# Performance work log

Measured on AMD Instinct MI355X. Metric: run time of the kernel, lower is better.

The kernel has to match this reference:

```python
import jax, jax.numpy as jnp
import numpy as np

SEM_DIM = 256
N_LEVELS = 21
HALF = jnp.float32((N_LEVELS - 1) / 2.0)  # 10.0
BETA = 0.1  # commitment cost


def setup_inputs() -> dict:
    key = jax.random.key(0)
    k1, k2 = jax.random.split(key)
    z = jax.random.normal(k1, (8, 292, 2048), dtype=jnp.float32)
    # nn.init.uniform_(codebook.weight, -1/dim, 1/dim)
    codebook = jax.random.uniform(k2, (8192, SEM_DIM), dtype=jnp.float32,
                                  minval=-1.0 / SEM_DIM, maxval=1.0 / SEM_DIM)
    return {"z": z, "codebook": codebook}


def reference(z, codebook):
    # Split latent: semantic (VQ) / acoustic (FSQ)
    z_sem = z[:, :SEM_DIM, :]   # (B, 256, T)
    z_ac = z[:, SEM_DIM:, :]    # (B, 36, T)
    B, D, T = z_sem.shape

    # ---- VectorQuantizer (eval path) ----
    z_flat = jnp.transpose(z_sem, (0, 2, 1)).reshape(B * T, D)  # (BT, D)
    # ||z||^2 - 2 z.c^T + ||c||^2
    dists = (jnp.sum(z_flat * z_flat, axis=1, keepdims=True)
             - 2.0 * jnp.einsum('nd,kd->nk', z_flat, codebook)
             + jnp.sum(codebook * codebook, axis=1)[None, :])  # (BT, K)
    indices = jnp.argmin(dists, axis=1)  # (BT,)
    z_q = codebook[indices].reshape(B, T, D).transpose(0, 2, 1)  # (B, D, T)

    codebook_loss = jnp.mean((z_q - jax.lax.stop_gradient(z_sem)) ** 2)
    commitment_loss = BETA * jnp.mean((jax.lax.stop_gradient(z_q) - z_sem) ** 2)
    vq_loss = codebook_loss + commitment_loss

    # straight-through
    z_sem_q = z_sem + jax.lax.stop_gradient(z_q - z_sem)

    # ---- FSQ quantize (eval path) ----
    z_b = jnp.tanh(z_ac) * HALF
    z_ac_q = z_b + jax.lax.stop_gradient(jnp.round(z_b) - z_b)  # round STE
    ac_codes = jnp.clip(jnp.round(z_ac_q + HALF).astype(jnp.int32), 0, N_LEVELS - 1)

    z_out = jnp.concatenate([z_sem_q, z_ac_q], axis=1)  # (B, 292, T)
    return z_out, indices.reshape(B, T), ac_codes, vq_loss, z_ac_q
```

## Files before the change

### kernel.cpp

```cpp
#include <hip/hip_runtime.h>
#include <cfloat>
#include <math.h>

#define BQ 8
#define T 2048
#define D 256
#define DAC 36
#define CH 292
#define K 8192
#define NROWS (BQ*T)
#define TAU 1e-3f
#define FSPLIT 4
#define RSPLIT 16
#define CAPROWS 8192

#define OFF_IDX   (BQ*CH*T)
#define OFF_CODES (OFF_IDX + NROWS)
#define OFF_LOSS  (OFF_CODES + BQ*DAC*T)
#define OFF_ACQ   (OFF_LOSS + 1)

#define WN_C2    0
#define WN_Z2    32768
#define WN_CNT   98304
#define WN_LIST  98560
#define WN_LOSS  164096
#define WN_WIDX  168192
#define WN_QCNT  233728
#define WN_PMX   262144
#define WN_PR    262144
#define WN_AZ    2359296
#define WN_ZG    2359296
#define WN_BC    10747904
#define WN_QL    14942208
#define WN_NEED  15204352

#define WS_C2    0
#define WS_Z2    32768
#define WS_PART  131072
#define WS_IDX   655360
#define WS_LOSS  720896
#define MT 32
#define KT 128
#define DC 32
#define NSPLIT 4

typedef float f32x4 __attribute__((ext_vector_type(4)));
typedef __bf16 bf16x8 __attribute__((ext_vector_type(8)));
typedef __attribute__((address_space(1))) const unsigned int gu32;
typedef __attribute__((address_space(3))) unsigned int lu32;

__device__ inline void gl_lds16(const void* gp, void* lp) {
    __builtin_amdgcn_global_load_lds((gu32*)gp, (lu32*)lp, 16, 0, 0);
}

__device__ inline unsigned short f2bf(float x) {
    unsigned u = __float_as_uint(x);
    return (unsigned short)((u + 0x7fffu + ((u >> 16) & 1u)) >> 16);
}

__device__ inline void merge3(float& m1, float& m2, int& mi, float o1, float o2, int oi) {
    if (o1 < m1 || (o1 == m1 && oi < mi)) { m2 = fminf(m1, o2); m1 = o1; mi = oi; }
    else                                  { m2 = fminf(m2, o1); }
}

template <typename F>
__device__ float np_pairwise256_sq(F ld) {
    float S[2];
    #pragma unroll
    for (int h = 0; h < 2; h++) {
        int base = h * 128;
        float v[16];
        #pragma unroll
        for (int l = 0; l < 16; l++) {
            float q[8];
            #pragma unroll
            for (int j = 0; j < 8; j++) { float x = ld(base + j * 16 + l); q[j] = x * x; }
            v[l] = ((q[0] + q[1]) + (q[2] + q[3])) + ((q[4] + q[5]) + (q[6] + q[7]));
        }
        float t1[8], t2[4], t3[2];
        #pragma unroll
        for (int l = 0; l < 8; l++) t1[l] = v[l] + v[l + 8];
        #pragma unroll
        for (int l = 0; l < 4; l++) t2[l] = t1[l] + t1[l + 4];
        t3[0] = t2[0] + t2[2]; t3[1] = t2[1] + t2[3];
        S[h] = t3[0] + t3[1];
    }
    return S[0] + S[1];
}

__global__ void k_c2pw(const float* __restrict__ cb, float* __restrict__ c2) {
    int k = blockIdx.x * 256 + threadIdx.x;
    const float* row = cb + (size_t)k * D;
    c2[k] = np_pairwise256_sq([&](int d) { return row[d]; });
}

__global__ void k_z2pw(const float* __restrict__ z, float* __restrict__ z2) {
    int n = blockIdx.x * 256 + threadIdx.x;
    int b = n >> 11, t = n & 2047;
    const float* base = z + (size_t)b * CH * T + t;
    z2[n] = np_pairwise256_sq([&](int d) { return base[(size_t)d * T]; });
}

__global__ __launch_bounds__(256) void k_prep(const float* __restrict__ z,
        const float* __restrict__ cb, unsigned short* __restrict__ Az,
        unsigned short* __restrict__ Bc, float* __restrict__ c2,
        float* __restrict__ z2, int* __restrict__ cnt, int* __restrict__ qcnt,
        float* __restrict__ out) {
    __shared__ float zt[32][260];
    const int tid = threadIdx.x;
    if ((int)blockIdx.x < (K / 4)) {
        const int w = tid >> 6, l = tid & 63;
        const int k = blockIdx.x * 4 + w;
        float4 v = *(const float4*)(cb + (size_t)k * D + l * 4);
        *(float4*)&zt[w][l * 4] = v;
        float fa[4] = {v.x, v.y, v.z, v.w};
        unsigned short hh[4];
        #pragma unroll
        for (int e = 0; e < 4; e++) hh[e] = f2bf(fa[e]);
        *(uint2*)(Bc + (size_t)k * 256 + l * 4) = *(uint2*)hh;
        __syncthreads();
        if (tid < 4) {
            int kk = blockIdx.x * 4 + tid;
            c2[kk] = np_pairwise256_sq([&](int d) { return zt[tid][d]; });
        }
        if (blockIdx.x == 0) {
            if (tid == 0) *cnt = 0;
            if (tid < 4) qcnt[tid] = 0;
        }
    } else if ((int)blockIdx.x < (K / 4) + 512) {
        const int bb = blockIdx.x - (K / 4);
        const int b = bb >> 6, t0 = (bb & 63) * 32;
        for (int i = tid; i < 2048; i += 256) {
            int d = i >> 3, tq = (i & 7) * 4;
            float4 v = *(const float4*)(z + (size_t)(b * CH + d) * T + t0 + tq);
            zt[tq + 0][d] = v.x; zt[tq + 1][d] = v.y;
            zt[tq + 2][d] = v.z; zt[tq + 3][d] = v.w;
        }
        __syncthreads();
        const int t = tid >> 3, c8 = tid & 7;
        unsigned short* rowp = Az + (size_t)(b * 2048 + t0 + t) * 256;
        #pragma unroll
        for (int li = 0; li < 4; li++) {
            int u = c8 + 8 * li;
            int dbase = u * 8;
            float f[8];
            *(float4*)&f[0] = *(float4*)&zt[t][dbase];
            *(float4*)&f[4] = *(float4*)&zt[t][dbase + 4];
            unsigned short h[8];
            #pragma unroll
            for (int e = 0; e < 8; e++) h[e] = f2bf(f[e]);
            *(uint4*)(rowp + u * 8) = *(uint4*)h;
        }
        if (tid < 32)
            z2[b * 2048 + t0 + tid] = np_pairwise256_sq([&](int d) { return zt[tid][d]; });
    } else {
        const int ab = blockIdx.x - ((K / 4) + 512);
        int i = (ab * 256 + tid) * 4;
        int b = i / (DAC * T);
        int r = i % (DAC * T);
        int d = r / T, t = r % T;
        size_t zoff = ((size_t)(b * CH + 256 + d)) * T + t;
        float4 v = *(const float4*)(z + zoff);
        float r0, r1, r2, r3;
        {
            float t0 = (float)tanh((double)v.x); r0 = rintf(t0 * 10.0f);
            float t1 = (float)tanh((double)v.y); r1 = rintf(t1 * 10.0f);
            float t2 = (float)tanh((double)v.z); r2 = rintf(t2 * 10.0f);
            float t3 = (float)tanh((double)v.w); r3 = rintf(t3 * 10.0f);
        }
        *(float4*)(out + zoff) = make_float4(r0, r1, r2, r3);
        size_t co = OFF_CODES + (size_t)(b * DAC + d) * T + t;
        *(float4*)(out + co) = make_float4(r0 + 10.0f, r1 + 10.0f, r2 + 10.0f, r3 + 10.0f);
        size_t ao = OFF_ACQ + (size_t)(b * DAC + d) * T + t;
        out[ao + 0] = r0; out[ao + 1] = r1; out[ao + 2] = r2; out[ao + 3] = r3;
    }
}

__global__ __launch_bounds__(256, 2) void k_fast(
        const unsigned short* __restrict__ Az, const unsigned short* __restrict__ Bc,
        const float* __restrict__ c2g, float4* __restrict__ pmx) {
    __shared__ __align__(16) unsigned char smem8[65536];
    __shared__ float c2s[2048];

    const int tid = threadIdx.x;
    const int w = tid >> 6, lane = tid & 63;
    const int quad = lane >> 4, c = lane & 15;

    const int sp = blockIdx.x >> 7;
    const int nt = blockIdx.x & 127;
    const int n0 = nt * 128;
    const int kbase = sp * 2048;

    const char* Azb = (const char*)Az;
    const char* Bcb = (const char*)Bc;

    #pragma unroll
    for (int i = 0; i < 8; i++) c2s[tid + i * 256] = c2g[kbase + tid + i * 256];

    const int hi2 = lane >> 5;
    const char* sq[8];
    #pragma unroll
    for (int q = 0; q < 8; q++) {
        const int seg = w * 8 + q;
        const int code = seg * 2 + hi2;
        sq[q] = Bcb + (size_t)(kbase + code) * 512 + (((lane & 31) ^ (code & 7)) << 4);
    }
    auto stage = [&](int t, int buf) {
        unsigned char* base = smem8 + buf * 32768;
        #pragma unroll
        for (int q = 0; q < 8; q++)
            gl_lds16(sq[q] + (size_t)t * 32768, base + (w * 8 + q) * 1024);
    };

    int voff[8];
    #pragma unroll
    for (int ks = 0; ks < 8; ks++)
        voff[ks] = c * 512 + (((((ks << 2) | quad) ^ (c & 7))) << 4);

    bf16x8 af[2][8];
    #pragma unroll
    for (int i = 0; i < 2; i++)
        #pragma unroll
        for (int ks = 0; ks < 8; ks++)
            af[i][ks] = *(const bf16x8*)(Azb +
                (size_t)(n0 + w * 32 + i * 16 + c) * 512 + ks * 64 + quad * 16);

    float bm1[8], bm2[8]; int bid[8];
    #pragma unroll
    for (int sl = 0; sl < 8; sl++) { bm1[sl] = FLT_MAX; bm2[sl] = FLT_MAX; bid[sl] = 0x7fffffff; }

    f32x4 accA[2][4], accB[2][4];

    #define MFMA_TILE(BUFC, ACC) do {                                         \
        _Pragma("unroll")                                                     \
        for (int i = 0; i < 2; i++)                                           \
            _Pragma("unroll")                                                 \
            for (int j = 0; j < 4; j++) ACC[i][j] = (f32x4)0.0f;              \
        __builtin_amdgcn_s_setprio(1);                                        \
        _Pragma("unroll")                                                     \
        for (int j = 0; j < 4; j++) {                                         \
            bf16x8 bf[8];                                                     \
            _Pragma("unroll")                                                 \
            for (int ks = 0; ks < 8; ks++)                                    \
                bf[ks] = *(const bf16x8*)(smem8 + voff[ks] +                  \
                                          ((BUFC) * 32768 + j * 8192));       \
            _Pragma("unroll")                                                 \
            for (int ks = 0; ks < 8; ks++) {                 \
                ACC[0][j] = __builtin_amdgcn_mfma_f32_16x16x32_bf16(af[0][ks], bf[ks], ACC[0][j], 0, 0, 0); \
                ACC[1][j] = __builtin_amdgcn_mfma_f32_16x16x32_bf16(af[1][ks], bf[ks], ACC[1][j], 0, 0, 0); \
            }                                                                 \
        }                                                                     \
        __builtin_amdgcn_s_setprio(0);                                        \
    } while (0)

    auto epilogue = [&](int t, f32x4 (&acc)[2][4]) {
        const int k0 = kbase + t * 64;
        #pragma unroll
        for (int j = 0; j < 4; j++) {
            const int kk = k0 + j * 16 + c;
            const float c2v = c2s[t * 64 + j * 16 + c];
            #pragma unroll
            for (int i = 0; i < 2; i++)
                #pragma unroll
                for (int r = 0; r < 4; r++) {
                    float sc = fmaf(-2.0f, acc[i][j][r], c2v);
                    int sl = i * 4 + r;
                    bm2[sl] = __builtin_amdgcn_fmed3f(bm1[sl], sc, bm2[sl]);
                    if (sc < bm1[sl]) { bm1[sl] = sc; bid[sl] = kk; }
                }
        }
    };

    stage(0, 0);
    __syncthreads();
    stage(1, 1);
    MFMA_TILE(0, accA);

    #define FITER(T, BUF, CUR, PRV) do {                                  \
        asm volatile("s_waitcnt vmcnt(0)" ::: "memory");                  \
        __builtin_amdgcn_s_barrier();                                     \
        __builtin_amdgcn_sched_barrier(0);                                \
        if ((T) < 31) stage((T) + 1, (BUF) ^ 1);                          \
        MFMA_TILE(BUF, CUR);                                              \
        epilogue((T) - 1, PRV);                                           \
    } while (0)

    for (int tt = 1; tt < 31; tt += 2) {
        FITER(tt,     1, accB, accA);
        FITER(tt + 1, 0, accA, accB);
    }
    FITER(31, 1, accB, accA);
    epilogue(31, accB);
    #undef FITER
    #undef MFMA_TILE

    #pragma unroll
    for (int mask = 1; mask <= 8; mask <<= 1)
        #pragma unroll
        for (int sl = 0; sl < 8; sl++) {
            float o1 = __shfl_xor(bm1[sl], mask, 64);
            float o2 = __shfl_xor(bm2[sl], mask, 64);
            int   oi = __shfl_xor(bid[sl], mask, 64);
            merge3(bm1[sl], bm2[sl], bid[sl], o1, o2, oi);
        }
    if (c == 0) {
        #pragma unroll
        for (int i = 0; i < 2; i++)
            #pragma unroll
            for (int r = 0; r < 4; r++) {
                int row = w * 32 + i * 16 + quad * 4 + r, sl = i * 4 + r;
                pmx[(size_t)sp * NROWS + n0 + row] =
                    make_float4(bm1[sl], bm2[sl], __int_as_float(bid[sl]), 0.f);
            }
    }
}

__global__ __launch_bounds__(256) void k_reduce2(const float4* __restrict__ pmx,
                          int* __restrict__ widx,
                          int* __restrict__ cnt, int* __restrict__ list,
                          float* __restrict__ out, const float* __restrict__ z,
                          float* __restrict__ zg, int* __restrict__ qcnt,
                          int* __restrict__ ql) {
    __shared__ int lrow[256], lpos[256];
    __shared__ int lcnt;
    const int tid = threadIdx.x;
    if (tid == 0) lcnt = 0;
    __syncthreads();
    int n = blockIdx.x * 256 + tid;
    float4 pv[FSPLIT];
    float a1 = FLT_MAX, a2 = FLT_MAX; int ai = 0x7fffffff;
    #pragma unroll
    for (int s = 0; s < FSPLIT; s++) {
        pv[s] = pmx[(size_t)s * NROWS + n];
        merge3(a1, a2, ai, pv[s].x, pv[s].y, __float_as_int(pv[s].z));
    }
    if (a2 - a1 < TAU) {
        int pos = atomicAdd(cnt, 1);
        list[pos] = n;
        int mask = 0;
        #pragma unroll
        for (int s = 0; s < FSPLIT; s++) {
            if (pv[s].x <= a1 + TAU) {
                mask |= 1 << s;
                int qp = atomicAdd(&qcnt[s], 1);
                ql[s * NROWS + qp] = pos;
            }
        }
        widx[n] = ~(pos | (mask << 14));
        int l = atomicAdd(&lcnt, 1);
        lrow[l] = n; lpos[l] = pos;
    } else {
        widx[n] = ai;
        out[OFF_IDX + n] = (float)ai;
    }
    __syncthreads();
    const int lc = lcnt;
    for (int it = 0; it < lc; it++) {
        int pos = lpos[it];
        if (pos < CAPROWS) {
            int rn = lrow[it];
            zg[(size_t)pos * D + tid] =
                z[((size_t)((rn >> 11) * CH + tid)) * T + (rn & 2047)];
        }
    }
}

__global__ __launch_bounds__(256, 2) void k_rescuex(
        const float* __restrict__ z, const float* __restrict__ cb,
        const float* __restrict__ c2, const float* __restrict__ z2,
        const int* __restrict__ list, const int* __restrict__ qcnt,
        const int* __restrict__ ql,
        const float* __restrict__ zg, float2* __restrict__ pr) {
    __shared__ float zs[D][MT + 4];
    __shared__ float cs[2][DC][KT + 4];
    __shared__ float c2s[512];
    __shared__ int   ls[MT];
    __shared__ int   lpo[MT];
    __shared__ float z2sh[MT];
    const int tid = threadIdx.x;
    const int tx = tid & 31, ty = tid >> 5;
    const int fs = blockIdx.x & 3, sub = (blockIdx.x >> 2) & 3;
    const int grp = blockIdx.x >> 4;
    const int qc = qcnt[fs];
    const int base = grp * MT;
    if (base >= qc) return;
    const int nr = min(MT, qc - base);
    const int kbase = fs * 2048 + sub * 512;
    const int rs = fs * 4 + sub;
    const int kl = tid & 127, half = tid >> 7;

    if (tid < MT) {
        int qi = base + ((tid < nr) ? tid : (nr - 1));
        int pos = ql[fs * NROWS + qi];
        int n = list[pos];
        ls[tid] = n; lpo[tid] = pos;
        z2sh[tid] = z2[n];
    }
    #pragma unroll
    for (int i = 0; i < 2; i++)
        c2s[tid + i * 256] = c2[kbase + tid + i * 256];

    float4 rv0, rv1, rv2, rv3;
    auto ldchunk = [&](int ch) {
        const int k0 = kbase + (ch >> 3) * KT, dcc = (ch & 7) * DC;
        const float4* src = (const float4*)(cb + (size_t)(k0 + kl) * D + dcc + half * 16);
        rv0 = src[0]; rv1 = src[1]; rv2 = src[2]; rv3 = src[3];
    };
    auto wrchunk = [&](int b) {
        const int dl = half * 16;
        cs[b][dl + 0][kl] = rv0.x; cs[b][dl + 1][kl] = rv0.y;
        cs[b][dl + 2][kl] = rv0.z; cs[b][dl + 3][kl] = rv0.w;
        cs[b][dl + 4][kl] = rv1.x; cs[b][dl + 5][kl] = rv1.y;
        cs[b][dl + 6][kl] = rv1.z; cs[b][dl + 7][kl] = rv1.w;
        cs[b][dl + 8][kl] = rv2.x; cs[b][dl + 9][kl] = rv2.y;
        cs[b][dl + 10][kl] = rv2.z; cs[b][dl + 11][kl] = rv2.w;
        cs[b][dl + 12][kl] = rv3.x; cs[b][dl + 13][kl] = rv3.y;
        cs[b][dl + 14][kl] = rv3.z; cs[b][dl + 15][kl] = rv3.w;
    };

    ldchunk(0);
    __syncthreads();
    for (int i = tid; i < MT * 64; i += 256) {
        int r = i >> 6, dq = (i & 63) << 2;
        int po = lpo[r];
        if (po < CAPROWS) {
            float4 v = *(const float4*)(zg + (size_t)po * D + dq);
            zs[dq + 0][r] = v.x; zs[dq + 1][r] = v.y;
            zs[dq + 2][r] = v.z; zs[dq + 3][r] = v.w;
        } else {
            int n = ls[r];
            #pragma unroll
            for (int e = 0; e < 4; e++)
                zs[dq + e][r] = z[((size_t)((n >> 11) * CH + dq + e)) * T + (n & 2047)];
        }
    }
    __syncthreads();
    wrchunk(0);
    ldchunk(1);
    asm volatile("s_waitcnt lgkmcnt(0)" ::: "memory");
    __builtin_amdgcn_s_barrier();
    __builtin_amdgcn_sched_barrier(0);

    float z2r[4];
    #pragma unroll
    for (int i = 0; i < 4; i++) z2r[i] = z2sh[ty * 4 + i];

    float m1[4]; int bi[4];
    #pragma unroll
    for (int i = 0; i < 4; i++) { m1[i] = FLT_MAX; bi[i] = 0x7fffffff; }
    float acc[4][4] = {};

    const int NCH = (512 / KT) * (D / DC);
    for (int ch = 0; ch < NCH; ch++) {
        const int b = ch & 1;
        const int dcc = (ch & 7) * DC;
        #pragma unroll 8
        for (int d = 0; d < DC; d++) {
            const float4 zf = *(const float4*)&zs[dcc + d][ty * 4];
            const float4 cf = *(const float4*)&cs[b][d][tx * 4];
            const float za[4] = {zf.x, zf.y, zf.z, zf.w};
            const float ca[4] = {cf.x, cf.y, cf.z, cf.w};
            #pragma unroll
            for (int i = 0; i < 4; i++)
                #pragma unroll
                for (int j = 0; j < 4; j++)
                    acc[i][j] = fmaf(za[i], ca[j], acc[i][j]);
        }
        if ((ch & 7) == 7) {
            const int koff = (ch >> 3) * KT;
            #pragma unroll
            for (int j = 0; j < 4; j++) {
                int kk = kbase + koff + tx * 4 + j;
                float c2v = c2s[koff + tx * 4 + j];
                #pragma unroll
                for (int i = 0; i < 4; i++) {
                    float tpre = z2r[i] - 2.0f * acc[i][j];
                    float s = tpre + c2v;
                    if (s < m1[i]) { m1[i] = s; bi[i] = kk; }
                }
            }
            #pragma unroll
            for (int i = 0; i < 4; i++)
                #pragma unroll
                for (int j = 0; j < 4; j++) acc[i][j] = 0.0f;
        }
        if (ch < NCH - 1) {
            __syncthreads();
            wrchunk(b ^ 1);
            if (ch < NCH - 2) ldchunk(ch + 2);
            asm volatile("s_waitcnt lgkmcnt(0)" ::: "memory");
            __builtin_amdgcn_s_barrier();
            __builtin_amdgcn_sched_barrier(0);
        }
    }
    __syncthreads();
    float* rm1 = (float*)zs;
    int*   rix = (int*)(rm1 + MT * 32);
    #pragma unroll
    for (int i = 0; i < 4; i++) {
        int slot = (ty * 4 + i) * 32 + tx;
        rm1[slot] = m1[i]; rix[slot] = bi[i];
    }
    __syncthreads();
    if (tid < MT) {
        float a1 = FLT_MAX; int ai = 0x7fffffff;
        for (int t = 0; t < 32; t++) {
            float b1 = rm1[tid * 32 + t]; int bidx = rix[tid * 32 + t];
            if (b1 < a1 || (b1 == a1 && bidx < ai)) { a1 = b1; ai = bidx; }
        }
        if (tid < nr)
            pr[(size_t)rs * NROWS + lpo[tid]] = make_float2(a1, __int_as_float(ai));
    }
}

__global__ __launch_bounds__(256) void k_exact(
        const float* __restrict__ z, const float* __restrict__ cb,
        const float* __restrict__ c2, const float* __restrict__ z2,
        float2* __restrict__ part) {
    __shared__ float zs[D][MT];
    __shared__ float cs[DC][KT + 4];
    const int tid = threadIdx.x;
    const int tx = tid & 31, ty = tid >> 5;
    const int n0 = blockIdx.x * MT;
    const int bb = n0 >> 11, t0 = n0 & 2047;
    const int kbase = blockIdx.y * (K / NSPLIT);
    for (int i = tid; i < D * (MT / 4); i += 256) {
        int d = i >> 3, tg = i & 7;
        float4 v = *(const float4*)(z + ((size_t)(bb * CH + d)) * T + t0 + tg * 4);
        *(float4*)&zs[d][tg * 4] = v;
    }
    float z2r[4];
    #pragma unroll
    for (int i = 0; i < 4; i++) z2r[i] = z2[n0 + ty * 4 + i];
    float m1[4]; int bi[4];
    #pragma unroll
    for (int i = 0; i < 4; i++) { m1[i] = FLT_MAX; bi[i] = 0x7fffffff; }
    for (int ktt = 0; ktt < K / NSPLIT; ktt += KT) {
        const int k0 = kbase + ktt;
        float acc[4][4] = {};
        for (int dc = 0; dc < D; dc += DC) {
            __syncthreads();
            {
                int kl = tid & 127, half = tid >> 7;
                const float4* src = (const float4*)(cb + (size_t)(k0 + kl) * D + dc + half * 16);
                #pragma unroll
                for (int j = 0; j < 4; j++) {
                    float4 v = src[j];
                    int dl = half * 16 + j * 4;
                    cs[dl + 0][kl] = v.x; cs[dl + 1][kl] = v.y;
                    cs[dl + 2][kl] = v.z; cs[dl + 3][kl] = v.w;
                }
            }
            __syncthreads();
            #pragma unroll 8
            for (int d = 0; d < DC; d++) {
                const float4 zf = *(const float4*)&zs[dc + d][ty * 4];
                const float4 cf = *(const float4*)&cs[d][tx * 4];
                const float za[4] = {zf.x, zf.y, zf.z, zf.w};
                const float ca[4] = {cf.x, cf.y, cf.z, cf.w};
                #pragma unroll
                for (int i = 0; i < 4; i++)
                    #pragma unroll
                    for (int j = 0; j < 4; j++)
                        acc[i][j] = fmaf(za[i], ca[j], acc[i][j]);
            }
        }
        #pragma unroll
        for (int j = 0; j < 4; j++) {
            int kk = k0 + tx * 4 + j;
            float c2v = c2[kk];
            #pragma unroll
            for (int i = 0; i < 4; i++) {
                float tpre = z2r[i] - 2.0f * acc[i][j];
                float s = tpre + c2v;
                if (s < m1[i]) { m1[i] = s; bi[i] = kk; }
            }
        }
    }
    __syncthreads();
    float* rm1 = (float*)zs;
    int*   rix = (int*)(rm1 + MT * 32);
    #pragma unroll
    for (int i = 0; i < 4; i++) {
        int slot = (ty * 4 + i) * 32 + tx;
        rm1[slot] = m1[i]; rix[slot] = bi[i];
    }
    __syncthreads();
    if (tid < MT) {
        float a1 = FLT_MAX; int ai = 0x7fffffff;
        for (int t = 0; t < 32; t++) {
            float b1 = rm1[tid * 32 + t]; int bidx = rix[tid * 32 + t];
            if (b1 < a1 || (b1 == a1 && bidx < ai)) { a1 = b1; ai = bidx; }
        }
        part[(size_t)(n0 + tid) * NSPLIT + blockIdx.y] = make_float2(a1, __int_as_float(ai));
    }
}

__global__ void k_reduce(const float2* __restrict__ part, int* __restrict__ widx,
                         float* __restrict__ out) {
    int n = blockIdx.x * 256 + threadIdx.x;
    float a1 = FLT_MAX; int ai = 0x7fffffff;
    #pragma unroll
    for (int s = 0; s < NSPLIT; s++) {
        float2 p = part[(size_t)n * NSPLIT + s];
        float b1 = p.x; int bidx = __float_as_int(p.y);
        if (b1 < a1 || (b1 == a1 && bidx < ai)) { a1 = b1; ai = bidx; }
    }
    widx[n] = ai;
    out[OFF_IDX + n] = (float)ai;
}

__global__ __launch_bounds__(256) void k_episem(
        const float* __restrict__ z, const float* __restrict__ cb,
        const int* __restrict__ widx, const float2* __restrict__ pr,
        float* __restrict__ out, double* __restrict__ lossp) {
    __shared__ int qidx[32];
    __shared__ float qs[32][260];
    __shared__ double wsum[4];
    const int tid = threadIdx.x;
    const int bb = blockIdx.x >> 6;
    const int t0 = (blockIdx.x & 63) * 32;
    if (tid < 32) {
        int n = bb * T + t0 + tid;
        int wv = widx[n];
        if (wv < 0) {
            unsigned u = ~wv;
            int pos = u & 16383;
            int mask = (u >> 14) & 15;
            float a1 = FLT_MAX; int ai = 0x7fffffff;
            #pragma unroll
            for (int s = 0; s < RSPLIT; s++) {
                if ((mask >> (s >> 2)) & 1) {
                    float2 p = pr[(size_t)s * NROWS + pos];
                    float v = p.x; int ix = __float_as_int(p.y);
                    if (v < a1 || (v == a1 && ix < ai)) { a1 = v; ai = ix; }
                }
            }
            wv = ai;
            out[OFF_IDX + n] = (float)ai;
        }
        qidx[tid] = wv;
    }
    __syncthreads();
    for (int i = tid; i < 32 * 64; i += 256) {
        int tl = i >> 6, lanee = i & 63;
        float4 v = *(const float4*)(cb + (size_t)qidx[tl] * D + lanee * 4);
        *(float4*)&qs[tl][lanee * 4] = v;
    }
    __syncthreads();
    double ls = 0.0;
    for (int it = 0; it < 32; it++) {
        int d = it * 8 + (tid >> 5);
        int tl = tid & 31;
        size_t ga = ((size_t)(bb * CH + d)) * T + t0 + tl;
        float q = qs[tl][d];
        float e = q - z[ga];
        out[ga] = q;
        ls += (double)e * (double)e;
    }
    #pragma unroll
    for (int off = 32; off; off >>= 1) ls += __shfl_down(ls, off, 64);
    if ((tid & 63) == 0) wsum[tid >> 6] = ls;
    __syncthreads();
    if (tid == 0) lossp[blockIdx.x] = wsum[0] + wsum[1] + wsum[2] + wsum[3];
}

__global__ void k_loss(const double* __restrict__ lossp, float* __restrict__ out) {
    __shared__ double sm[256];
    int tid = threadIdx.x;
    sm[tid] = lossp[tid] + lossp[tid + 256];
    __syncthreads();
    for (int off = 128; off; off >>= 1) {
        if (tid < off) sm[tid] += sm[tid + off];
        __syncthreads();
    }
    if (tid == 0) out[OFF_LOSS] = (float)(1.1 * sm[0] / (double)(BQ * D * T));
}

__global__ __launch_bounds__(256) void k_episemf(
        const float* __restrict__ z, const float* __restrict__ cb,
        const int* __restrict__ widx, float* __restrict__ out, double* __restrict__ lossp) {
    __shared__ int qidx[32];
    __shared__ float qs[32][260];
    __shared__ double wsum[4];
    const int tid = threadIdx.x;
    const int bb = blockIdx.x >> 6;
    const int t0 = (blockIdx.x & 63) * 32;
    if (tid < 32) qidx[tid] = widx[bb * T + t0 + tid];
    __syncthreads();
    for (int i = tid; i < 32 * 64; i += 256) {
        int tl = i >> 6, lanee = i & 63;
        float4 v = *(const float4*)(cb + (size_t)qidx[tl] * D + lanee * 4);
        *(float4*)&qs[tl][lanee * 4] = v;
    }
    __syncthreads();
    double ls = 0.0;
    for (int it = 0; it < 32; it++) {
        int d = it * 8 + (tid >> 5);
        int tl = tid & 31;
        size_t ga = ((size_t)(bb * CH + d)) * T + t0 + tl;
        float q = qs[tl][d];
        float e = q - z[ga];
        out[ga] = q;
        ls += (double)e * (double)e;
    }
    #pragma unroll
    for (int off = 32; off; off >>= 1) ls += __shfl_down(ls, off, 64);
    if ((tid & 63) == 0) wsum[tid >> 6] = ls;
    __syncthreads();
    if (tid == 0) lossp[blockIdx.x] = wsum[0] + wsum[1] + wsum[2] + wsum[3];
}

__global__ void k_epiac(const float* __restrict__ z, const double* __restrict__ lossp,
                        float* __restrict__ out) {
    __shared__ double sm[256];
    int i = (blockIdx.x * 256 + threadIdx.x) * 4;
    int b = i / (DAC * T);
    int r = i % (DAC * T);
    int d = r / T, t = r % T;
    size_t zoff = ((size_t)(b * CH + 256 + d)) * T + t;
    float4 v = *(const float4*)(z + zoff);
    float r0, r1, r2, r3;
    {
        float t0 = (float)tanh((double)v.x); r0 = rintf(t0 * 10.0f);
        float t1 = (float)tanh((double)v.y); r1 = rintf(t1 * 10.0f);
        float t2 = (float)tanh((double)v.z); r2 = rintf(t2 * 10.0f);
        float t3 = (float)tanh((double)v.w); r3 = rintf(t3 * 10.0f);
    }
    *(float4*)(out + zoff) = make_float4(r0, r1, r2, r3);
    size_t co = OFF_CODES + (size_t)(b * DAC + d) * T + t;
    *(float4*)(out + co) = make_float4(r0 + 10.0f, r1 + 10.0f, r2 + 10.0f, r3 + 10.0f);
    size_t ao = OFF_ACQ + (size_t)(b * DAC + d) * T + t;
    out[ao + 0] = r0; out[ao + 1] = r1; out[ao + 2] = r2; out[ao + 3] = r3;
    if (blockIdx.x == 0) {
        int tid = threadIdx.x;
        sm[tid] = lossp[tid] + lossp[tid + 256];
        __syncthreads();
        for (int off = 128; off; off >>= 1) {
            if (tid < off) sm[tid] += sm[tid + off];
            __syncthreads();
        }
        if (tid == 0) out[OFF_LOSS] = (float)(1.1 * sm[0] / (double)(BQ * D * T));
    }
}

extern "C" void kernel_launch(void* const* d_in, const int* in_sizes, int n_in,
                              void* d_out, int out_size, void* d_ws, size_t ws_size,
                              hipStream_t stream) {
    const float* z  = (const float*)d_in[0];
    const float* cb = (const float*)d_in[1];
    float* out = (float*)d_out;
    char* ws = (char*)d_ws;

    if (ws_size >= (size_t)WN_NEED) {
        float*  c2    = (float*)(ws + WN_C2);
        float*  z2    = (float*)(ws + WN_Z2);
        int*    cnt   = (int*)(ws + WN_CNT);
        int*    list  = (int*)(ws + WN_LIST);
        double* lossp = (double*)(ws + WN_LOSS);
        int*    widx  = (int*)(ws + WN_WIDX);
        int*    qcnt  = (int*)(ws + WN_QCNT);
        int*    ql    = (int*)(ws + WN_QL);
        float4* pmx   = (float4*)(ws + WN_PMX);
        unsigned short* Az = (unsigned short*)(ws + WN_AZ);
        unsigned short* Bc = (unsigned short*)(ws + WN_BC);
        float*  zg    = (float*)(ws + WN_ZG);
        float2* pr    = (float2*)(ws + WN_PR);

        hipLaunchKernelGGL(k_prep,    dim3(K / 4 + 512 + BQ * DAC * T / 1024), dim3(256), 0, stream,
                           z, cb, Az, Bc, c2, z2, cnt, qcnt, out);
        hipLaunchKernelGGL(k_fast,    dim3(128 * FSPLIT), dim3(256), 0, stream, Az, Bc, c2, pmx);
        hipLaunchKernelGGL(k_reduce2, dim3(NROWS / 256),  dim3(256), 0, stream,
                           pmx, widx, cnt, list, out, z, zg, qcnt, ql);
        hipLaunchKernelGGL(k_rescuex, dim3((NROWS / MT) * RSPLIT), dim3(256), 0, stream,
                           z, cb, c2, z2, list, qcnt, ql, zg, pr);
        hipLaunchKernelGGL(k_episem,  dim3(BQ * (T / 32)), dim3(256), 0, stream,
                           z, cb, widx, pr, out, lossp);
        hipLaunchKernelGGL(k_loss,    dim3(1),            dim3(256), 0, stream, lossp, out);
    } else {
        float*  c2    = (float*)(ws + WS_C2);
        float*  z2    = (float*)(ws + WS_Z2);
        float2* part  = (float2*)(ws + WS_PART);
        int*    widx  = (int*)(ws + WS_IDX);
        double* lossp = (double*)(ws + WS_LOSS);
        hipLaunchKernelGGL(k_c2pw,   dim3(K / 256),            dim3(256), 0, stream, cb, c2);
        hipLaunchKernelGGL(k_z2pw,   dim3(NROWS / 256),        dim3(256), 0, stream, z, z2);
        hipLaunchKernelGGL(k_exact,  dim3(NROWS / MT, NSPLIT), dim3(256), 0, stream, z, cb, c2, z2, part);
        hipLaunchKernelGGL(k_reduce, dim3(NROWS / 256),        dim3(256), 0, stream, part, widx, out);
        hipLaunchKernelGGL(k_episemf, dim3(BQ * (T / 32)),     dim3(256), 0, stream, z, cb, widx, out, lossp);
        hipLaunchKernelGGL(k_epiac,  dim3(BQ * DAC * T / 1024), dim3(256), 0, stream, z, lossp, out);
    }
}
```

Measured before the change: 255.0 us.

## Fuse split-K argmin reduction into k_fast via last-block-done counters

The separate k_reduce2 launch is removed. Each k_fast block now bumps a per-row-tile atomic counter after writing its partial best-two candidates, and the last of the four split blocks merges them, builds the ambiguous-row rescue lists and gathers z rows. This saves a kernel launch and a round trip of the partials through memory, at the cost of threadfences, an extra atomic per block, and the reduction tail running in only one of four blocks. The zg gather buffer moves to its own workspace region, since it can no longer alias the still-live Az, and the gather cap is lowered to 768 rows to fit.

```diff
diff --git a/kernel.cpp b/kernel.cpp
--- a/kernel.cpp
+++ b/kernel.cpp
@@ -12,7 +12,7 @@
 #define TAU 1e-3f
 #define FSPLIT 4
 #define RSPLIT 16
-#define CAPROWS 8192
+#define CAPROWS 768
 
 #define OFF_IDX   (BQ*CH*T)
 #define OFF_CODES (OFF_IDX + NROWS)
@@ -26,13 +26,14 @@
 #define WN_LOSS  164096
 #define WN_WIDX  168192
 #define WN_QCNT  233728
+#define WN_NTC   233744
 #define WN_PMX   262144
 #define WN_PR    262144
 #define WN_AZ    2359296
-#define WN_ZG    2359296
 #define WN_BC    10747904
 #define WN_QL    14942208
-#define WN_NEED  15204352
+#define WN_ZG    15204352
+#define WN_NEED  15990784
 
 #define WS_C2    0
 #define WS_Z2    32768
@@ -105,7 +106,7 @@
         const float* __restrict__ cb, unsigned short* __restrict__ Az,
         unsigned short* __restrict__ Bc, float* __restrict__ c2,
         float* __restrict__ z2, int* __restrict__ cnt, int* __restrict__ qcnt,
-        float* __restrict__ out) {
+        int* __restrict__ ntc, float* __restrict__ out) {
     __shared__ float zt[32][260];
     const int tid = threadIdx.x;
     if ((int)blockIdx.x < (K / 4)) {
@@ -126,6 +127,7 @@
         if (blockIdx.x == 0) {
             if (tid == 0) *cnt = 0;
             if (tid < 4) qcnt[tid] = 0;
+            if (tid < 128) ntc[tid] = 0;
         }
     } else if ((int)blockIdx.x < (K / 4) + 512) {
         const int bb = blockIdx.x - (K / 4);
@@ -178,9 +180,15 @@
 
 __global__ __launch_bounds__(256, 2) void k_fast(
         const unsigned short* __restrict__ Az, const unsigned short* __restrict__ Bc,
-        const float* __restrict__ c2g, float4* __restrict__ pmx) {
+        const float* __restrict__ c2g, float4* pmx,
+        const float* __restrict__ z, float* __restrict__ out,
+        int* __restrict__ widx, int* __restrict__ cnt, int* __restrict__ list,
+        int* __restrict__ qcnt, int* __restrict__ ql, int* __restrict__ ntcnt,
+        float* __restrict__ zg) {
     __shared__ __align__(16) unsigned char smem8[65536];
     __shared__ float c2s[2048];
+    __shared__ int lrow[128], lpos[128];
+    __shared__ int lcnt2, lred;
 
     const int tid = threadIdx.x;
     const int w = tid >> 6, lane = tid & 63;
@@ -313,52 +321,50 @@
                     make_float4(bm1[sl], bm2[sl], __int_as_float(bid[sl]), 0.f);
             }
     }
-}
-
-__global__ __launch_bounds__(256) void k_reduce2(const float4* __restrict__ pmx,
-                          int* __restrict__ widx,
-                          int* __restrict__ cnt, int* __restrict__ list,
-                          float* __restrict__ out, const float* __restrict__ z,
-                          float* __restrict__ zg, int* __restrict__ qcnt,
-                          int* __restrict__ ql) {
-    __shared__ int lrow[256], lpos[256];
-    __shared__ int lcnt;
-    const int tid = threadIdx.x;
-    if (tid == 0) lcnt = 0;
-    __syncthreads();
-    int n = blockIdx.x * 256 + tid;
-    float4 pv[FSPLIT];
-    float a1 = FLT_MAX, a2 = FLT_MAX; int ai = 0x7fffffff;
-    #pragma unroll
-    for (int s = 0; s < FSPLIT; s++) {
-        pv[s] = pmx[(size_t)s * NROWS + n];
-        merge3(a1, a2, ai, pv[s].x, pv[s].y, __float_as_int(pv[s].z));
-    }
-    if (a2 - a1 < TAU) {
-        int pos = atomicAdd(cnt, 1);
-        list[pos] = n;
-        int mask = 0;
+
+    __threadfence();
+    if (tid == 0) {
+        lred = (atomicAdd(&ntcnt[nt], 1) == 3);
+        lcnt2 = 0;
+    }
+    __syncthreads();
+    if (!lred) return;
+    __threadfence();
+    if (tid < 128) {
+        int n = n0 + tid;
+        float4 pv[FSPLIT];
+        float a1 = FLT_MAX, a2 = FLT_MAX; int ai = 0x7fffffff;
         #pragma unroll
         for (int s = 0; s < FSPLIT; s++) {
-            if (pv[s].x <= a1 + TAU) {
-                mask |= 1 << s;
-                int qp = atomicAdd(&qcnt[s], 1);
-                ql[s * NROWS + qp] = pos;
+            pv[s] = pmx[(size_t)s * NROWS + n];
+            merge3(a1, a2, ai, pv[s].x, pv[s].y, __float_as_int(pv[s].z));
+        }
+        if (a2 - a1 < TAU) {
+            int pos = atomicAdd(cnt, 1);
+            list[pos] = n;
+            int mask = 0;
+            #pragma unroll
+            for (int s = 0; s < FSPLIT; s++) {
+                if (pv[s].x <= a1 + TAU) {
+                    mask |= 1 << s;
+                    int qp = atomicAdd(&qcnt[s], 1);
+                    ql[s * NROWS + qp] = pos;
+                }
             }
-        }
-        widx[n] = ~(pos | (mask << 14));
-        int l = atomicAdd(&lcnt, 1);
-        lrow[l] = n; lpos[l] = pos;
-    } else {
-        widx[n] = ai;
-        out[OFF_IDX + n] = (float)ai;
-    }
-    __syncthreads();
-    const int lc = lcnt;
-    for (int it = 0; it < lc; it++) {
-        int pos = lpos[it];
+            widx[n] = ~(pos | (mask << 14));
+            int l = atomicAdd(&lcnt2, 1);
+            lrow[l] = n; lpos[l] = pos;
+        } else {
+            widx[n] = ai;
+            out[OFF_IDX + n] = (float)ai;
+        }
+    }
+    __syncthreads();
+    const int lc = lcnt2;
+    for (int it2 = 0; it2 < lc; it2++) {
+        int pos = lpos[it2];
         if (pos < CAPROWS) {
-            int rn = lrow[it];
+            int rn = lrow[it2];
             zg[(size_t)pos * D + tid] =
                 z[((size_t)((rn >> 11) * CH + tid)) * T + (rn & 2047)];
         }
@@ -760,6 +766,7 @@
         double* lossp = (double*)(ws + WN_LOSS);
         int*    widx  = (int*)(ws + WN_WIDX);
         int*    qcnt  = (int*)(ws + WN_QCNT);
+        int*    ntc   = (int*)(ws + WN_NTC);
         int*    ql    = (int*)(ws + WN_QL);
         float4* pmx   = (float4*)(ws + WN_PMX);
         unsigned short* Az = (unsigned short*)(ws + WN_AZ);
@@ -768,10 +775,9 @@
         float2* pr    = (float2*)(ws + WN_PR);
 
         hipLaunchKernelGGL(k_prep,    dim3(K / 4 + 512 + BQ * DAC * T / 1024), dim3(256), 0, stream,
-                           z, cb, Az, Bc, c2, z2, cnt, qcnt, out);
-        hipLaunchKernelGGL(k_fast,    dim3(128 * FSPLIT), dim3(256), 0, stream, Az, Bc, c2, pmx);
-        hipLaunchKernelGGL(k_reduce2, dim3(NROWS / 256),  dim3(256), 0, stream,
-                           pmx, widx, cnt, list, out, z, zg, qcnt, ql);
+                           z, cb, Az, Bc, c2, z2, cnt, qcnt, ntc, out);
+        hipLaunchKernelGGL(k_fast,    dim3(128 * FSPLIT), dim3(256), 0, stream,
+                           Az, Bc, c2, pmx, z, out, widx, cnt, list, qcnt, ql, ntc, zg);
         hipLaunchKernelGGL(k_rescuex, dim3((NROWS / MT) * RSPLIT), dim3(256), 0, stream,
                            z, cb, c2, z2, list, qcnt, ql, zg, pr);
         hipLaunchKernelGGL(k_episem,  dim3(BQ * (T / 32)), dim3(256), 0, stream,
```

Result: slower. 294.6 us (+15.5%).
